# Kernel tuning notes

Measured on AMD Instinct MI355X. Metric: run time of the kernel, lower is better.

Reference implementation:

```python
import jax, jax.numpy as jnp
import numpy as np

# sign with straight-through estimator: grad passes only where |input| < 1
@jax.custom_vjp
def sign_ste(x):
    return jnp.sign(x)

def _sign_ste_fwd(x):
    return jnp.sign(x), x

def _sign_ste_bwd(x, g):
    return (jnp.where(jnp.abs(x) < 1.0, g, jnp.zeros_like(g)),)

sign_ste.defvjp(_sign_ste_fwd, _sign_ste_bwd)

# weight binarization: torch mutates weight.data in-place, so autograd treats
# sign() as identity w.r.t. the weight variable (plain linear gradient)
@jax.custom_vjp
def sign_id(w):
    return jnp.sign(w)

def _sign_id_fwd(w):
    return jnp.sign(w), None

def _sign_id_bwd(_, g):
    return (g,)

sign_id.defvjp(_sign_id_fwd, _sign_id_bwd)


def setup_inputs() -> dict:
    key = jax.random.key(0)
    k1, k2, k3 = jax.random.split(key, 3)
    x = jax.random.normal(k1, (8192, 4096), dtype=jnp.float32)
    # weight initialized to random ±1 (bernoulli(0.5)*2-1), as in __init__
    W = jnp.sign(jax.random.normal(k2, (4096, 4096), dtype=jnp.float32))
    b = jax.random.normal(k3, (4096,), dtype=jnp.float32) * 0.02
    return {"x": x, "W": W, "b": b}


def reference(x, W, b):
    # x: [N, in]; W: [out, in]; b: [out]
    x_mean = jnp.mean(jnp.abs(x))          # scalar scale, differentiable
    xb = sign_ste(x)                        # ±1 activations, STE gradient
    wb = sign_id(W)                         # ±1 weights, identity gradient
    out = jnp.einsum('ni,oi->no', xb, wb) + b  # [N, out]
    return out * x_mean
```

## Files before the change

kernel.cpp:

```cpp
#include <hip/hip_runtime.h>

typedef int intx4 __attribute__((ext_vector_type(4)));

#define M_DIM 8192
#define N_DIM 4096
#define K_DIM 4096

__device__ __forceinline__ void gld_lds16(const char* g, char* l) {
  __builtin_amdgcn_global_load_lds(
      (const __attribute__((address_space(1))) unsigned int*)g,
      (__attribute__((address_space(3))) unsigned int*)l,
      16, 0, 0);
}

__device__ __forceinline__ unsigned sgn_byte(float v) {
  return (unsigned)(unsigned char)(char)((v > 0.0f) - (v < 0.0f));
}

__device__ __forceinline__ float pack16(const float* src, int* dst) {
  float s = 0.0f;
  int4 o;
  int* op = (int*)&o;
  #pragma unroll
  for (int q = 0; q < 4; ++q) {
    float4 v = ((const float4*)src)[q];
    op[q] = (int)(sgn_byte(v.x) | (sgn_byte(v.y) << 8) |
                  (sgn_byte(v.z) << 16) | (sgn_byte(v.w) << 24));
    s += fabsf(v.x) + fabsf(v.y) + fabsf(v.z) + fabsf(v.w);
  }
  *(int4*)dst = o;
  return s;
}

__global__ __launch_bounds__(256) void pack_x_kernel(const float* __restrict__ x,
                                                     char* __restrict__ xb,
                                                     double* __restrict__ accd) {
  const int t = threadIdx.x;
  const int lane = t & 63;
  const int w = t >> 6;
  size_t tid = (size_t)blockIdx.x * blockDim.x + t;
  size_t stride = (size_t)gridDim.x * blockDim.x;
  const size_t nchunk = (size_t)M_DIM * K_DIM / 16;
  float s = 0.0f;
  for (size_t c = tid; c < nchunk; c += stride)
    s += pack16(x + c * 16, (int*)(xb + c * 16));
  #pragma unroll
  for (int off = 32; off > 0; off >>= 1) s += __shfl_down(s, off);
  __shared__ float part[4];
  if (lane == 0) part[w] = s;
  __syncthreads();
  if (t == 0) atomicAdd(accd, (double)(part[0] + part[1] + part[2] + part[3]));
}

__global__ __launch_bounds__(256) void pack_w_kernel(const float* __restrict__ Wm,
                                                     char* __restrict__ wb) {
  size_t tid = (size_t)blockIdx.x * blockDim.x + threadIdx.x;
  size_t stride = (size_t)gridDim.x * blockDim.x;
  const size_t nchunk = (size_t)N_DIM * K_DIM / 16;
  for (size_t c = tid; c < nchunk; c += stride) {
    const float* src = Wm + c * 16;
    int* dst = (int*)(wb + c * 16);
    int4 o;
    int* op = (int*)&o;
    #pragma unroll
    for (int q = 0; q < 4; ++q) {
      float4 v = ((const float4*)src)[q];
      op[q] = (int)(sgn_byte(v.x) | (sgn_byte(v.y) << 8) |
                    (sgn_byte(v.z) << 16) | (sgn_byte(v.w) << 24));
    }
    *(int4*)dst = o;
  }
}

__global__ __launch_bounds__(256) void gemm_kernel(const char* __restrict__ Xb,
                                                   const char* __restrict__ Wb,
                                                   const float* __restrict__ bias,
                                                   const double* __restrict__ accd,
                                                   float* __restrict__ out) {
  __shared__ __align__(16) char ldsA[128 * 128];
  __shared__ __align__(16) char ldsB[128 * 128];
  const int t = threadIdx.x;
  const int lane = t & 63;
  const int w = t >> 6;
  const int m16 = lane & 15;
  const int quad = lane >> 4;
  const int bM = blockIdx.y * 128;
  const int bN = blockIdx.x * 128;
  const int waveM = (w & 1) * 64;
  const int waveN = (w >> 1) * 64;
  const int srow = t >> 3;
  const int schunk = t & 7;

  intx4 acc[4][4];
  #pragma unroll
  for (int i = 0; i < 4; ++i)
    #pragma unroll
    for (int j = 0; j < 4; ++j)
      acc[i][j] = (intx4){0, 0, 0, 0};

  for (int kt = 0; kt < K_DIM; kt += 128) {
    __syncthreads();
    #pragma unroll
    for (int i = 0; i < 4; ++i) {
      const int r = srow + 32 * i;
      const int g = (schunk + r) & 7;
      gld_lds16(Xb + (size_t)(bM + r) * K_DIM + kt + g * 16,
                ldsA + (size_t)(32 * i + 8 * w) * 128);
      gld_lds16(Wb + (size_t)(bN + r) * K_DIM + kt + g * 16,
                ldsB + (size_t)(32 * i + 8 * w) * 128);
    }
    __syncthreads();

    #pragma unroll
    for (int s = 0; s < 2; ++s) {
      intx4 a[4], b[4];
      #pragma unroll
      for (int i = 0; i < 4; ++i) {
        const int r = waveM + i * 16 + m16;
        const int c = ((s * 4 + quad) - r) & 7;
        a[i] = *(const intx4*)&ldsA[r * 128 + c * 16];
      }
      #pragma unroll
      for (int j = 0; j < 4; ++j) {
        const int r = waveN + j * 16 + m16;
        const int c = ((s * 4 + quad) - r) & 7;
        b[j] = *(const intx4*)&ldsB[r * 128 + c * 16];
      }
      #pragma unroll
      for (int i = 0; i < 4; ++i)
        #pragma unroll
        for (int j = 0; j < 4; ++j)
          acc[i][j] = __builtin_amdgcn_mfma_i32_16x16x64_i8(a[i], b[j], acc[i][j], 0, 0, 0);
    }
  }

  const float scale = (float)(*accd * (1.0 / (double)((size_t)M_DIM * K_DIM)));

  #pragma unroll
  for (int j = 0; j < 4; ++j) {
    const int col = bN + waveN + j * 16 + m16;
    const float bj = bias[col];
    #pragma unroll
    for (int i = 0; i < 4; ++i) {
      const size_t row0 = (size_t)(bM + waveM + i * 16 + quad * 4);
      float* po = out + row0 * N_DIM + col;
      #pragma unroll
      for (int r = 0; r < 4; ++r)
        po[(size_t)r * N_DIM] = ((float)acc[i][j][r] + bj) * scale;
    }
  }
}

extern "C" void kernel_launch(void* const* d_in, const int* in_sizes, int n_in,
                              void* d_out, int out_size, void* d_ws, size_t ws_size,
                              hipStream_t stream) {
  const float* x = (const float*)d_in[0];
  const float* W = (const float*)d_in[1];
  const float* b = (const float*)d_in[2];
  float* out = (float*)d_out;

  double* accd = (double*)d_ws;
  char* Xb = (char*)d_ws + 256;
  char* Wb = (char*)d_ws + 256 + (size_t)M_DIM * K_DIM;

  hipMemsetAsync(d_ws, 0, 8, stream);
  pack_x_kernel<<<4096, 256, 0, stream>>>(x, Xb, accd);
  pack_w_kernel<<<2048, 256, 0, stream>>>(W, Wb);
  gemm_kernel<<<dim3(N_DIM / 128, M_DIM / 128), 256, 0, stream>>>(Xb, Wb, b, accd, out);
}
```

Baseline: 428.1 us.

## Pack signs as FP4 nibbles and use scaled f8f6f4 MFMA, merge pack kernels

Binarized activations and weights are now packed as 4-bit FP4 values (±1.0 or 0) instead of int8, which halves the packed workspace and the GEMM's global and LDS traffic. The GEMM switches to the MI355X mfma_scale_f32_16x16x128_f8f6f4 instruction in FP4 mode with unit scales, accumulating in fp32. The two pack kernels are merged into a single launch that splits its blocks between x and W. Each FP4 operand fills only half of the 8-register input, with the upper half zero-padded, and the LDS layout and swizzle are redone for the narrower rows.

```diff
diff --git a/kernel.cpp b/kernel.cpp
--- a/kernel.cpp
+++ b/kernel.cpp
@@ -1,10 +1,13 @@
 #include <hip/hip_runtime.h>
 
 typedef int intx4 __attribute__((ext_vector_type(4)));
+typedef int intx8 __attribute__((ext_vector_type(8)));
+typedef float floatx4 __attribute__((ext_vector_type(4)));
 
 #define M_DIM 8192
 #define N_DIM 4096
 #define K_DIM 4096
+#define KB2 (K_DIM / 2)
 
 __device__ __forceinline__ void gld_lds16(const char* g, char* l) {
   __builtin_amdgcn_global_load_lds(
@@ -13,62 +16,50 @@
       16, 0, 0);
 }
 
-__device__ __forceinline__ unsigned sgn_byte(float v) {
-  return (unsigned)(unsigned char)(char)((v > 0.0f) - (v < 0.0f));
+__device__ __forceinline__ unsigned nib(float v) {
+  return v > 0.0f ? 0x2u : (v < 0.0f ? 0xAu : 0x0u);
 }
 
-__device__ __forceinline__ float pack16(const float* src, int* dst) {
+__device__ __forceinline__ float pack32(const float* __restrict__ src, int4* __restrict__ dst) {
   float s = 0.0f;
   int4 o;
   int* op = (int*)&o;
   #pragma unroll
   for (int q = 0; q < 4; ++q) {
-    float4 v = ((const float4*)src)[q];
-    op[q] = (int)(sgn_byte(v.x) | (sgn_byte(v.y) << 8) |
-                  (sgn_byte(v.z) << 16) | (sgn_byte(v.w) << 24));
-    s += fabsf(v.x) + fabsf(v.y) + fabsf(v.z) + fabsf(v.w);
+    float4 v0 = ((const float4*)src)[2 * q];
+    float4 v1 = ((const float4*)src)[2 * q + 1];
+    op[q] = (int)(nib(v0.x) | (nib(v0.y) << 4) | (nib(v0.z) << 8) | (nib(v0.w) << 12) |
+                  (nib(v1.x) << 16) | (nib(v1.y) << 20) | (nib(v1.z) << 24) | (nib(v1.w) << 28));
+    s += fabsf(v0.x) + fabsf(v0.y) + fabsf(v0.z) + fabsf(v0.w)
+       + fabsf(v1.x) + fabsf(v1.y) + fabsf(v1.z) + fabsf(v1.w);
   }
-  *(int4*)dst = o;
+  *dst = o;
   return s;
 }
 
-__global__ __launch_bounds__(256) void pack_x_kernel(const float* __restrict__ x,
-                                                     char* __restrict__ xb,
-                                                     double* __restrict__ accd) {
+__global__ __launch_bounds__(256) void pack_kernel(const float* __restrict__ x,
+                                                   const float* __restrict__ Wm,
+                                                   char* __restrict__ xb,
+                                                   char* __restrict__ wb,
+                                                   double* __restrict__ accd) {
   const int t = threadIdx.x;
-  const int lane = t & 63;
-  const int w = t >> 6;
-  size_t tid = (size_t)blockIdx.x * blockDim.x + t;
-  size_t stride = (size_t)gridDim.x * blockDim.x;
-  const size_t nchunk = (size_t)M_DIM * K_DIM / 16;
-  float s = 0.0f;
-  for (size_t c = tid; c < nchunk; c += stride)
-    s += pack16(x + c * 16, (int*)(xb + c * 16));
-  #pragma unroll
-  for (int off = 32; off > 0; off >>= 1) s += __shfl_down(s, off);
-  __shared__ float part[4];
-  if (lane == 0) part[w] = s;
-  __syncthreads();
-  if (t == 0) atomicAdd(accd, (double)(part[0] + part[1] + part[2] + part[3]));
-}
-
-__global__ __launch_bounds__(256) void pack_w_kernel(const float* __restrict__ Wm,
-                                                     char* __restrict__ wb) {
-  size_t tid = (size_t)blockIdx.x * blockDim.x + threadIdx.x;
-  size_t stride = (size_t)gridDim.x * blockDim.x;
-  const size_t nchunk = (size_t)N_DIM * K_DIM / 16;
-  for (size_t c = tid; c < nchunk; c += stride) {
-    const float* src = Wm + c * 16;
-    int* dst = (int*)(wb + c * 16);
-    int4 o;
-    int* op = (int*)&o;
+  if (blockIdx.x < 2048) {
+    const size_t nch = (size_t)M_DIM * K_DIM / 32;
+    size_t tid = (size_t)blockIdx.x * 256 + t;
+    float s = 0.0f;
+    for (size_t c = tid; c < nch; c += (size_t)2048 * 256)
+      s += pack32(x + c * 32, (int4*)(xb + c * 16));
     #pragma unroll
-    for (int q = 0; q < 4; ++q) {
-      float4 v = ((const float4*)src)[q];
-      op[q] = (int)(sgn_byte(v.x) | (sgn_byte(v.y) << 8) |
-                    (sgn_byte(v.z) << 16) | (sgn_byte(v.w) << 24));
-    }
-    *(int4*)dst = o;
+    for (int off = 32; off > 0; off >>= 1) s += __shfl_down(s, off);
+    __shared__ float part[4];
+    if ((t & 63) == 0) part[t >> 6] = s;
+    __syncthreads();
+    if (t == 0) atomicAdd(accd, (double)(part[0] + part[1] + part[2] + part[3]));
+  } else {
+    const size_t nch = (size_t)N_DIM * K_DIM / 32;
+    size_t tid = (size_t)(blockIdx.x - 2048) * 256 + t;
+    for (size_t c = tid; c < nch; c += (size_t)1024 * 256)
+      pack32(Wm + c * 32, (int4*)(wb + c * 16));
   }
 }
 
@@ -77,8 +68,8 @@
                                                    const float* __restrict__ bias,
                                                    const double* __restrict__ accd,
                                                    float* __restrict__ out) {
-  __shared__ __align__(16) char ldsA[128 * 128];
-  __shared__ __align__(16) char ldsB[128 * 128];
+  __shared__ __align__(16) char ldsA[128 * 64];
+  __shared__ __align__(16) char ldsB[128 * 64];
   const int t = threadIdx.x;
   const int lane = t & 63;
   const int w = t >> 6;
@@ -88,49 +79,49 @@
   const int bN = blockIdx.x * 128;
   const int waveM = (w & 1) * 64;
   const int waveN = (w >> 1) * 64;
-  const int srow = t >> 3;
-  const int schunk = t & 7;
+  const int srl = 2 * (t >> 3) + (t & 1);
+  const int ssc = (t >> 1) & 3;
 
-  intx4 acc[4][4];
+  floatx4 acc[4][4];
   #pragma unroll
   for (int i = 0; i < 4; ++i)
     #pragma unroll
     for (int j = 0; j < 4; ++j)
-      acc[i][j] = (intx4){0, 0, 0, 0};
+      acc[i][j] = (floatx4){0.0f, 0.0f, 0.0f, 0.0f};
 
   for (int kt = 0; kt < K_DIM; kt += 128) {
     __syncthreads();
     #pragma unroll
-    for (int i = 0; i < 4; ++i) {
-      const int r = srow + 32 * i;
-      const int g = (schunk + r) & 7;
-      gld_lds16(Xb + (size_t)(bM + r) * K_DIM + kt + g * 16,
-                ldsA + (size_t)(32 * i + 8 * w) * 128);
-      gld_lds16(Wb + (size_t)(bN + r) * K_DIM + kt + g * 16,
-                ldsB + (size_t)(32 * i + 8 * w) * 128);
+    for (int rd = 0; rd < 2; ++rd) {
+      const int r = rd * 64 + srl;
+      const int g = (ssc + (r >> 1)) & 3;
+      const size_t goff = (size_t)(kt >> 1) + g * 16;
+      gld_lds16(Xb + (size_t)(bM + r) * KB2 + goff, ldsA + rd * 4096 + w * 1024);
+      gld_lds16(Wb + (size_t)(bN + r) * KB2 + goff, ldsB + rd * 4096 + w * 1024);
     }
     __syncthreads();
 
+    intx8 a8[4];
     #pragma unroll
-    for (int s = 0; s < 2; ++s) {
-      intx4 a[4], b[4];
-      #pragma unroll
-      for (int i = 0; i < 4; ++i) {
-        const int r = waveM + i * 16 + m16;
-        const int c = ((s * 4 + quad) - r) & 7;
-        a[i] = *(const intx4*)&ldsA[r * 128 + c * 16];
-      }
-      #pragma unroll
-      for (int j = 0; j < 4; ++j) {
-        const int r = waveN + j * 16 + m16;
-        const int c = ((s * 4 + quad) - r) & 7;
-        b[j] = *(const intx4*)&ldsB[r * 128 + c * 16];
-      }
+    for (int i = 0; i < 4; ++i) {
+      const int m = waveM + i * 16 + m16;
+      const int c = (quad - (m >> 1)) & 3;
+      intx4 lo = *(const intx4*)&ldsA[(m >> 1) * 128 + c * 32 + (m & 1) * 16];
+      a8[i] = (intx8){lo[0], lo[1], lo[2], lo[3], 0, 0, 0, 0};
+    }
+    #pragma unroll
+    for (int j = 0; j < 4; ++j) {
+      const int n = waveN + j * 16 + m16;
+      const int c = (quad - (n >> 1)) & 3;
+      intx4 lo = *(const intx4*)&ldsB[(n >> 1) * 128 + c * 32 + (n & 1) * 16];
+      intx8 b8 = (intx8){lo[0], lo[1], lo[2], lo[3], 0, 0, 0, 0};
       #pragma unroll
       for (int i = 0; i < 4; ++i)
-        #pragma unroll
-        for (int j = 0; j < 4; ++j)
-          acc[i][j] = __builtin_amdgcn_mfma_i32_16x16x64_i8(a[i], b[j], acc[i][j], 0, 0, 0);
+        acc[i][j] = __builtin_amdgcn_mfma_scale_f32_16x16x128_f8f6f4(
+            a8[i], b8, acc[i][j],
+            4, 4,
+            0, 0x7F7F7F7F,
+            0, 0x7F7F7F7F);
     }
   }
 
@@ -146,7 +137,7 @@
       float* po = out + row0 * N_DIM + col;
       #pragma unroll
       for (int r = 0; r < 4; ++r)
-        po[(size_t)r * N_DIM] = ((float)acc[i][j][r] + bj) * scale;
+        po[(size_t)r * N_DIM] = (acc[i][j][r] + bj) * scale;
     }
   }
 }
@@ -161,10 +152,9 @@
 
   double* accd = (double*)d_ws;
   char* Xb = (char*)d_ws + 256;
-  char* Wb = (char*)d_ws + 256 + (size_t)M_DIM * K_DIM;
+  char* Wb = (char*)d_ws + 256 + (size_t)M_DIM * K_DIM / 2;
 
   hipMemsetAsync(d_ws, 0, 8, stream);
-  pack_x_kernel<<<4096, 256, 0, stream>>>(x, Xb, accd);
-  pack_w_kernel<<<2048, 256, 0, stream>>>(W, Wb);
+  pack_kernel<<<3072, 256, 0, stream>>>(x, W, Xb, Wb, accd);
   gemm_kernel<<<dim3(N_DIM / 128, M_DIM / 128), 256, 0, stream>>>(Xb, Wb, b, accd, out);
 }
```

Measured after the change: 350.7 us. 18.1% less time.
